# Performance work log

Hardware: AMD Instinct MI355X
Metric: run time of the kernel (lower is better)

The kernel has to match this reference:

```python
import jax, jax.numpy as jnp
import numpy as np

DIM = 512
HEADS = 8        # MultiHeadAttention default heads=8 (init 'heads' arg actually sets dim_head)
DIM_HEAD = 64    # from AttentionLayers heads=64 passed positionally as dim_head
HIDDEN = HEADS * DIM_HEAD  # 512
EPS = 1e-5


def setup_inputs() -> dict:
    key = jax.random.key(0)
    ks = jax.random.split(key, 8)
    s = 1.0 / np.sqrt(DIM)
    return {
        "x": jax.random.normal(ks[0], (4, 2048, DIM), dtype=jnp.float32),
        "ln_g": jnp.ones((DIM,), dtype=jnp.float32),
        "ln_b": jnp.zeros((DIM,), dtype=jnp.float32),
        "Wq": jax.random.normal(ks[1], (DIM, HIDDEN), dtype=jnp.float32) * s,
        "Wk": jax.random.normal(ks[2], (DIM, HIDDEN), dtype=jnp.float32) * s,
        "Wv": jax.random.normal(ks[3], (DIM, HIDDEN), dtype=jnp.float32) * s,
        "Wo": jax.random.normal(ks[4], (HIDDEN, DIM), dtype=jnp.float32) * s,
        "bo": jnp.zeros((DIM,), dtype=jnp.float32),
    }


def reference(x, ln_g, ln_b, Wq, Wk, Wv, Wo, bo):
    b, n, d = x.shape
    residual = x
    # pre-norm LayerNorm
    mu = jnp.mean(x, axis=-1, keepdims=True)
    var = jnp.mean((x - mu) ** 2, axis=-1, keepdims=True)
    xn = (x - mu) * jax.lax.rsqrt(var + EPS) * ln_g + ln_b
    # QKV projections (no bias), split into heads: [b, s, h, dh]
    q = (xn @ Wq).reshape(b, n, HEADS, DIM_HEAD)
    k = (xn @ Wk).reshape(b, n, HEADS, DIM_HEAD)
    v = (xn @ Wv).reshape(b, n, HEADS, DIM_HEAD)
    scale = HIDDEN ** (-0.5)  # note: scales by hidden_dim, not dim_head (faithful)
    scores = jnp.einsum('bihd,bjhd->bhij', q, k) * scale  # [b,h,i,j] full matrix
    attn = jax.nn.softmax(scores, axis=-1)
    out = jnp.einsum('bhij,bjhd->bihd', attn, v).reshape(b, n, HIDDEN)
    out = out @ Wo + bo
    # residual; the subsequent FFN layer's output is discarded in the source
    return out + residual
```

## Files before the change

kernel.cpp:

```cpp
#include <hip/hip_runtime.h>
#include <hip/hip_bf16.h>

#define DIM 512
#define SEQ 2048
#define BATCH 4
#define NHEADS 8
#define DH 64
#define NROWS (BATCH * SEQ)
#define LN_EPS 1e-5f

typedef __hip_bfloat16 bf16;
typedef __attribute__((ext_vector_type(8))) short short8;
typedef __attribute__((ext_vector_type(4))) float f32x4;

#define MFMA16(a, b, c) __builtin_amdgcn_mfma_f32_16x16x32_bf16((a), (b), (c), 0, 0, 0)

#if __has_builtin(__builtin_amdgcn_exp2f)
#define EXP2(x) __builtin_amdgcn_exp2f(x)
#else
#define EXP2(x) exp2f(x)
#endif

#if defined(__has_builtin)
#if __has_builtin(__builtin_amdgcn_global_load_lds)
#define HAS_GLDS 1
#endif
#endif

__device__ __forceinline__ void glds16(const bf16* g, bf16* l) {
#ifdef HAS_GLDS
  __builtin_amdgcn_global_load_lds((const __attribute__((address_space(1))) void*)g,
                                   (__attribute__((address_space(3))) void*)l, 16, 0, 0);
#else
  *reinterpret_cast<uint4*>(l) = *reinterpret_cast<const uint4*>(g);
#endif
}

__device__ __forceinline__ void store_bf16x4(bf16* p, float a, float b, float c, float d) {
  bf16 tmp[4] = {__float2bfloat16(a), __float2bfloat16(b), __float2bfloat16(c),
                 __float2bfloat16(d)};
  *reinterpret_cast<ushort4*>(p) = *reinterpret_cast<const ushort4*>(tmp);
}

#define B2F(us) __uint_as_float(((unsigned)(us)) << 16)

#define BARRIER() asm volatile("s_barrier" ::: "memory")
#define WAITVM0() asm volatile("s_waitcnt vmcnt(0)" ::: "memory")

#define Q_SCALE_LOG2E 0.06375872f

__global__ void setup_kernel(const float* __restrict__ x, const float* __restrict__ gamma,
                             const float* __restrict__ beta, bf16* __restrict__ xn,
                             const float* __restrict__ Wq, const float* __restrict__ Wk,
                             const float* __restrict__ Wv, const float* __restrict__ Wo,
                             bf16* __restrict__ Wt) {
  const int t = threadIdx.x;
  if (blockIdx.x < NROWS / 4) {
    const int row = blockIdx.x * 4 + (t >> 6);
    const int l = t & 63;
    const float4* xr = reinterpret_cast<const float4*>(x + (size_t)row * DIM);
    const float4 v0 = xr[l * 2];
    const float4 v1 = xr[l * 2 + 1];
    float s = (v0.x + v0.y + v0.z + v0.w) + (v1.x + v1.y + v1.z + v1.w);
    float ss = v0.x * v0.x + v0.y * v0.y + v0.z * v0.z + v0.w * v0.w + v1.x * v1.x +
               v1.y * v1.y + v1.z * v1.z + v1.w * v1.w;
#pragma unroll
    for (int off = 1; off < 64; off <<= 1) {
      s += __shfl_xor(s, off);
      ss += __shfl_xor(ss, off);
    }
    const float mu = s * (1.0f / DIM);
    const float rs = rsqrtf(ss * (1.0f / DIM) - mu * mu + LN_EPS);
    const float4 g0 = reinterpret_cast<const float4*>(gamma)[l * 2];
    const float4 g1 = reinterpret_cast<const float4*>(gamma)[l * 2 + 1];
    const float4 b0 = reinterpret_cast<const float4*>(beta)[l * 2];
    const float4 b1 = reinterpret_cast<const float4*>(beta)[l * 2 + 1];
    bf16* o = xn + (size_t)row * DIM + l * 8;
    store_bf16x4(o, (v0.x - mu) * rs * g0.x + b0.x, (v0.y - mu) * rs * g0.y + b0.y,
                 (v0.z - mu) * rs * g0.z + b0.z, (v0.w - mu) * rs * g0.w + b0.w);
    store_bf16x4(o + 4, (v1.x - mu) * rs * g1.x + b1.x, (v1.y - mu) * rs * g1.y + b1.y,
                 (v1.z - mu) * rs * g1.z + b1.z, (v1.w - mu) * rs * g1.w + b1.w);
  } else {
    __shared__ float tile[32][33];
    const int idx = blockIdx.x - NROWS / 4;
    const int bx = idx & 15, by = (idx >> 4) & 15, z = idx >> 8;
    const float* __restrict__ W = (z == 0) ? Wq : (z == 1) ? Wk : (z == 2) ? Wv : Wo;
    const float scale = (z == 0) ? Q_SCALE_LOG2E : 1.0f;
    bf16* __restrict__ dst = Wt + (size_t)z * DIM * DIM;
    const int tx = t & 31, ty = t >> 5;
#pragma unroll
    for (int i = 0; i < 32; i += 8)
      tile[ty + i][tx] = W[(size_t)(by * 32 + ty + i) * DIM + bx * 32 + tx];
    __syncthreads();
#pragma unroll
    for (int i = 0; i < 32; i += 8)
      dst[(size_t)(bx * 32 + ty + i) * DIM + by * 32 + tx] =
          __float2bfloat16(tile[tx][ty + i] * scale);
  }
}

__launch_bounds__(256, 3)
__global__ void gemm_qkv_kernel(const bf16* __restrict__ A, const bf16* __restrict__ Bt,
                                bf16* __restrict__ qo, bf16* __restrict__ ko,
                                bf16* __restrict__ vto) {
  const int m0 = blockIdx.x * 128, n0g = blockIdx.y * 128;
  __shared__ __align__(16) bf16 sA[2][128 * 32];
  __shared__ __align__(16) bf16 sB[2][128 * 32];
  const int t = threadIdx.x, w = t >> 6, l = t & 63;
  const int r = l & 15, g = l >> 4;
  const int wm = w >> 1, wn = w & 1;
  const int crow = w * 32 + (l >> 2);
  const int ccol = (l & 3) * 8;
  const bf16* gA = A + (size_t)(m0 + crow) * DIM + ccol;
  const bf16* gB = Bt + (size_t)(n0g + crow) * DIM + ccol;
  const int loff = l * 8;
  f32x4 acc[4][4] = {};
  glds16(gA, &sA[0][w * 1024 + loff]);
  glds16(gA + 16 * DIM, &sA[0][w * 1024 + loff + 512]);
  glds16(gB, &sB[0][w * 1024 + loff]);
  glds16(gB + 16 * DIM, &sB[0][w * 1024 + loff + 512]);
  const int NK = DIM / 32;
  const int z = n0g >> 9;
  const int b = m0 / SEQ;
  if (z != 2) {
    for (int ks = 0; ks < NK; ks++) {
      const int cur = ks & 1;
      __syncthreads();
      if (ks + 1 < NK) {
        const int k0n = (ks + 1) * 32;
        glds16(gA + k0n, &sA[1 - cur][w * 1024 + loff]);
        glds16(gA + 16 * DIM + k0n, &sA[1 - cur][w * 1024 + loff + 512]);
        glds16(gB + k0n, &sB[1 - cur][w * 1024 + loff]);
        glds16(gB + 16 * DIM + k0n, &sB[1 - cur][w * 1024 + loff + 512]);
      }
      short8 af[4], bfv[4];
#pragma unroll
      for (int i = 0; i < 4; i++)
        af[i] = *reinterpret_cast<const short8*>(&sA[cur][(wm * 64 + i * 16 + r) * 32 + g * 8]);
#pragma unroll
      for (int j = 0; j < 4; j++)
        bfv[j] = *reinterpret_cast<const short8*>(&sB[cur][(wn * 64 + j * 16 + r) * 32 + g * 8]);
#pragma unroll
      for (int i = 0; i < 4; i++)
#pragma unroll
        for (int j = 0; j < 4; j++) acc[i][j] = MFMA16(bfv[j], af[i], acc[i][j]);
    }
    bf16* __restrict__ outp = (z == 0) ? qo : ko;
    const int nc0 = (n0g & 511) + wn * 64;
#pragma unroll
    for (int i = 0; i < 4; i++) {
      const size_t mrow = (size_t)(m0 + wm * 64 + i * 16 + r) * DIM;
#pragma unroll
      for (int j = 0; j < 4; j++)
        store_bf16x4(outp + mrow + nc0 + j * 16 + g * 4, acc[i][j][0], acc[i][j][1],
                     acc[i][j][2], acc[i][j][3]);
    }
  } else {
    for (int ks = 0; ks < NK; ks++) {
      const int cur = ks & 1;
      __syncthreads();
      if (ks + 1 < NK) {
        const int k0n = (ks + 1) * 32;
        glds16(gA + k0n, &sA[1 - cur][w * 1024 + loff]);
        glds16(gA + 16 * DIM + k0n, &sA[1 - cur][w * 1024 + loff + 512]);
        glds16(gB + k0n, &sB[1 - cur][w * 1024 + loff]);
        glds16(gB + 16 * DIM + k0n, &sB[1 - cur][w * 1024 + loff + 512]);
      }
      short8 af[4], bfv[4];
#pragma unroll
      for (int i = 0; i < 4; i++)
        af[i] = *reinterpret_cast<const short8*>(&sA[cur][(wm * 64 + i * 16 + r) * 32 + g * 8]);
#pragma unroll
      for (int j = 0; j < 4; j++)
        bfv[j] = *reinterpret_cast<const short8*>(&sB[cur][(wn * 64 + j * 16 + r) * 32 + g * 8]);
#pragma unroll
      for (int i = 0; i < 4; i++)
#pragma unroll
        for (int j = 0; j < 4; j++) acc[i][j] = MFMA16(af[i], bfv[j], acc[i][j]);
    }
    const int nc0 = (n0g & 511) + wn * 64;
    const int seqbase = (m0 - b * SEQ) + wm * 64;
#pragma unroll
    for (int j = 0; j < 4; j++) {
      bf16* dst = vto + ((size_t)(b * DIM) + nc0 + j * 16 + r) * SEQ + seqbase + g * 4;
#pragma unroll
      for (int i = 0; i < 4; i++)
        store_bf16x4(dst + i * 16, acc[i][j][0], acc[i][j][1], acc[i][j][2], acc[i][j][3]);
    }
  }
}

template <bool SPLIT>
__launch_bounds__(256, 4)
__global__ void attn_kernel(const bf16* __restrict__ q, const bf16* __restrict__ k,
                            const bf16* __restrict__ vt, bf16* __restrict__ opart,
                            float* __restrict__ lpart) {
  const int bh = blockIdx.x, jh = blockIdx.y, it = blockIdx.z;
  const int b = bh >> 3, h = bh & 7;
  const int t = threadIdx.x, wv = t >> 6, l = t & 63;
  const int r = l & 15, g = l >> 4;
  __shared__ __align__(16) bf16 sK[2][32 * 64];
  __shared__ __align__(16) bf16 sV[2][64 * 32];
  __shared__ __align__(16) bf16 sPt[4][2][16][72];
  const int i0 = it * 128 + wv * 32;
  const bf16* qp = q + ((size_t)(b * SEQ) + i0 + r) * DIM + h * DH;
  short8 qf[2][2];
#pragma unroll
  for (int s = 0; s < 2; s++)
#pragma unroll
    for (int kc = 0; kc < 2; kc++)
      qf[s][kc] = *reinterpret_cast<const short8*>(qp + s * 16 * DIM + kc * 32 + g * 8);
  f32x4 oacc[2][4] = {};
  float lsum[2] = {0.f, 0.f};
  const int jbase = SPLIT ? jh * (SEQ / 2) : 0;
  const int kr8 = l >> 3;
  const int ku = ((l & 7) - kr8) & 7;
  const bf16* kg = k + ((size_t)(b * SEQ) + jbase + wv * 8 + kr8) * DIM + h * DH + ku * 8;
  const int vr4 = l >> 2;
  const int vu = ((l & 3) - ((l >> 3) & 3)) & 3;
  const bf16* vg = vt + ((size_t)(b * DIM) + h * DH + wv * 16 + vr4) * SEQ + jbase + vu * 8;
  const int loff = wv * 512 + l * 8;
  glds16(kg, &sK[0][loff]);
  glds16(vg, &sV[0][loff]);
  const int ek0 = r * 64 + 8 * ((g + r) & 7);
  const int ek1 = r * 64 + 8 * ((g + 4 + r) & 7);
  const int ev = r * 32 + 8 * ((g + (r >> 1)) & 3);
  const int NJ = (SPLIT ? SEQ / 2 : SEQ) / 32;
  for (int jt = 0; jt < NJ; jt++) {
    WAITVM0();
    BARRIER();
    if (jt + 1 < NJ) {
      const int j0n = (jt + 1) * 32;
      const int bn = (jt + 1) & 1;
      glds16(kg + (size_t)j0n * DIM, &sK[bn][loff]);
      glds16(vg + j0n, &sV[bn][loff]);
    }
    const bf16* sKb = sK[jt & 1];
    const bf16* sVb = sV[jt & 1];
    f32x4 st[2][2];
#pragma unroll
    for (int c = 0; c < 2; c++) {
      const short8 kf0 = *reinterpret_cast<const short8*>(sKb + 1024 * c + ek0);
      const short8 kf1 = *reinterpret_cast<const short8*>(sKb + 1024 * c + ek1);
#pragma unroll
      for (int s = 0; s < 2; s++) {
        f32x4 a = {0.f, 0.f, 0.f, 0.f};
        a = MFMA16(kf0, qf[s][0], a);
        a = MFMA16(kf1, qf[s][1], a);
        st[s][c] = a;
      }
    }
#pragma unroll
    for (int s = 0; s < 2; s++)
#pragma unroll
      for (int c = 0; c < 2; c++) {
        const float p0 = EXP2(st[s][c][0]);
        const float p1 = EXP2(st[s][c][1]);
        const float p2 = EXP2(st[s][c][2]);
        const float p3 = EXP2(st[s][c][3]);
        lsum[s] += (p0 + p1) + (p2 + p3);
        store_bf16x4(&sPt[wv][s][r][c * 16 + g * 4], p0, p1, p2, p3);
      }
    short8 pf[2];
#pragma unroll
    for (int s = 0; s < 2; s++)
      pf[s] = *reinterpret_cast<const short8*>(&sPt[wv][s][r][g * 8]);
#pragma unroll
    for (int dt = 0; dt < 4; dt++) {
      const short8 vf = *reinterpret_cast<const short8*>(sVb + 512 * dt + ev);
#pragma unroll
      for (int s = 0; s < 2; s++) oacc[s][dt] = MFMA16(vf, pf[s], oacc[s][dt]);
    }
  }
#pragma unroll
  for (int s = 0; s < 2; s++) {
    lsum[s] += __shfl_xor(lsum[s], 16);
    lsum[s] += __shfl_xor(lsum[s], 32);
  }
  const size_t obase = ((size_t)(SPLIT ? jh * 32 : 0) + bh) * SEQ;
#pragma unroll
  for (int s = 0; s < 2; s++) {
    const int i = i0 + s * 16 + r;
    if (l < 16) lpart[obase + i] = lsum[s];
#pragma unroll
    for (int dt = 0; dt < 4; dt++)
      store_bf16x4(opart + (obase + i) * 64 + dt * 16 + g * 4, oacc[s][dt][0], oacc[s][dt][1],
                   oacc[s][dt][2], oacc[s][dt][3]);
  }
  if (!SPLIT) {
    const size_t obase1 = ((size_t)32 + bh) * SEQ;
#pragma unroll
    for (int s = 0; s < 2; s++) {
      const int i = i0 + s * 16 + r;
      if (l < 16) lpart[obase1 + i] = 0.f;
#pragma unroll
      for (int dt = 0; dt < 4; dt++)
        store_bf16x4(opart + (obase1 + i) * 64 + dt * 16 + g * 4, 0.f, 0.f, 0.f, 0.f);
    }
  }
}

__launch_bounds__(256, 4)
__global__ void gemm_proj_kernel(const bf16* __restrict__ opart, const float* __restrict__ lpart,
                                 const bf16* __restrict__ Bt, const float* __restrict__ bo,
                                 const float* __restrict__ x, float* __restrict__ out) {
  const int m0 = blockIdx.x * 64, n0 = blockIdx.y * 128;
  __shared__ __align__(16) bf16 sA[64 * 32];
  __shared__ __align__(16) bf16 sB[128 * 32];
  const int t = threadIdx.x, w = t >> 6, l = t & 63;
  const int r = l & 15, g = l >> 4;
  const int wm = w >> 1, wn = w & 1;
  const int arow = t >> 2;
  const int acol = (t & 3) * 8;
  const bf16* gB = Bt + (size_t)(n0 + w * 32 + (l >> 2)) * DIM + (l & 3) * 8;
  f32x4 acc[2][4] = {};
  const int NK = DIM / 32;
  for (int ks = 0; ks < NK; ks++) {
    const int k0 = ks * 32;
    const int h = k0 >> 6;
    const int d0 = (k0 & 63) + acol;
    const int m = m0 + arow;
    const int bb = m >> 11, ii = m & 2047;
    const size_t row0 = ((size_t)(bb * 8 + h)) * SEQ + ii;
    const size_t row1 = row0 + (size_t)32 * SEQ;
    const uint4 A0 = *reinterpret_cast<const uint4*>(opart + row0 * 64 + d0);
    const uint4 A1 = *reinterpret_cast<const uint4*>(opart + row1 * 64 + d0);
    const float inv = 1.0f / (lpart[row0] + lpart[row1]);
    const ushort* a0 = (const ushort*)&A0;
    const ushort* a1 = (const ushort*)&A1;
    bf16 rr[8];
#pragma unroll
    for (int e = 0; e < 8; e++)
      rr[e] = __float2bfloat16((B2F(a0[e]) + B2F(a1[e])) * inv);
    const uint4 areg = *reinterpret_cast<const uint4*>(rr);
    __syncthreads();
    *reinterpret_cast<uint4*>(&sA[arow * 32 + acol]) = areg;
    glds16(gB + k0, sB + w * 1024 + l * 8);
    glds16(gB + 16 * DIM + k0, sB + w * 1024 + 512 + l * 8);
    __syncthreads();
    short8 af[2], bfv[4];
#pragma unroll
    for (int i = 0; i < 2; i++)
      af[i] = *reinterpret_cast<const short8*>(&sA[(wm * 32 + i * 16 + r) * 32 + g * 8]);
#pragma unroll
    for (int j = 0; j < 4; j++)
      bfv[j] = *reinterpret_cast<const short8*>(&sB[(wn * 64 + j * 16 + r) * 32 + g * 8]);
#pragma unroll
    for (int i = 0; i < 2; i++)
#pragma unroll
      for (int j = 0; j < 4; j++) acc[i][j] = MFMA16(bfv[j], af[i], acc[i][j]);
  }
#pragma unroll
  for (int i = 0; i < 2; i++) {
    const size_t mrow = (size_t)(m0 + wm * 32 + i * 16 + r) * DIM;
#pragma unroll
    for (int j = 0; j < 4; j++) {
      const int col0 = n0 + wn * 64 + j * 16 + g * 4;
      const float4 xb = *reinterpret_cast<const float4*>(x + mrow + col0);
      const float4 bb = *reinterpret_cast<const float4*>(bo + col0);
      float4 o;
      o.x = acc[i][j][0] + bb.x + xb.x;
      o.y = acc[i][j][1] + bb.y + xb.y;
      o.z = acc[i][j][2] + bb.z + xb.z;
      o.w = acc[i][j][3] + bb.w + xb.w;
      *reinterpret_cast<float4*>(out + mrow + col0) = o;
    }
  }
}

extern "C" void kernel_launch(void* const* d_in, const int* in_sizes, int n_in,
                              void* d_out, int out_size, void* d_ws, size_t ws_size,
                              hipStream_t stream) {
  (void)in_sizes; (void)n_in; (void)out_size;
  const float* x    = (const float*)d_in[0];
  const float* ln_g = (const float*)d_in[1];
  const float* ln_b = (const float*)d_in[2];
  const float* Wq   = (const float*)d_in[3];
  const float* Wk   = (const float*)d_in[4];
  const float* Wv   = (const float*)d_in[5];
  const float* Wo   = (const float*)d_in[6];
  const float* bo   = (const float*)d_in[7];
  float* out = (float*)d_out;
  char* ws = (char*)d_ws;
  bf16* xn  = (bf16*)(ws);
  bf16* wt  = (bf16*)(ws + (8u << 20));
  bf16* qb  = (bf16*)(ws + (10u << 20));
  bf16* kb  = (bf16*)(ws + (18u << 20));
  bf16* vtb = (bf16*)(ws + (26u << 20));
  bf16* opart = (bf16*)(ws + (34u << 20));
  float* lpart = (float*)(ws + (50u << 20));
  const bool split = ws_size >= ((50u << 20) + (1u << 19));

  setup_kernel<<<NROWS / 4 + 1024, 256, 0, stream>>>(x, ln_g, ln_b, xn, Wq, Wk, Wv, Wo, wt);
  gemm_qkv_kernel<<<dim3(NROWS / 128, (3 * DIM) / 128), 256, 0, stream>>>(xn, wt, qb, kb, vtb);
  if (split) {
    attn_kernel<true><<<dim3(BATCH * NHEADS, 2, SEQ / 128), 256, 0, stream>>>(
        qb, kb, vtb, opart, lpart);
  } else {
    attn_kernel<false><<<dim3(BATCH * NHEADS, 1, SEQ / 128), 256, 0, stream>>>(
        qb, kb, vtb, opart, lpart);
  }
  gemm_proj_kernel<<<dim3(NROWS / 64, DIM / 128), 256, 0, stream>>>(
      opart, lpart, wt + 3 * DIM * DIM, bo, x, out);
}
```

Baseline: 164.4 us.

## Triple-buffer QKV GEMM and double-buffer projection GEMM with register prefetch

The QKV GEMM moves from a double-buffered LDS pipeline to a triple-buffered one. It uses explicit vmcnt waits and one barrier per k-step, so global-to-LDS loads run two stages ahead. The output projection GEMM gains double-buffered LDS and register prefetch of the split-attention partials two steps ahead, with the combine written into the next buffer after the MFMAs. This drops one of its two barriers per k-step. The cost is more LDS per block, which may lower occupancy, and vmcnt counting that must stay correct for the glds instructions.

Measured after the change: 162.3 us. Within noise of the previous version (-1.3%).

```diff
diff --git a/kernel.cpp b/kernel.cpp
--- a/kernel.cpp
+++ b/kernel.cpp
@@ -46,6 +46,9 @@
 
 #define BARRIER() asm volatile("s_barrier" ::: "memory")
 #define WAITVM0() asm volatile("s_waitcnt vmcnt(0)" ::: "memory")
+#define WAITVM4() asm volatile("s_waitcnt vmcnt(4)" ::: "memory")
+#define WAITVM4_LGKM0() asm volatile("s_waitcnt vmcnt(4) lgkmcnt(0)" ::: "memory")
+#define WAITVM0_LGKM0() asm volatile("s_waitcnt vmcnt(0) lgkmcnt(0)" ::: "memory")
 
 #define Q_SCALE_LOG2E 0.06375872f
 
@@ -104,8 +107,8 @@
                                 bf16* __restrict__ qo, bf16* __restrict__ ko,
                                 bf16* __restrict__ vto) {
   const int m0 = blockIdx.x * 128, n0g = blockIdx.y * 128;
-  __shared__ __align__(16) bf16 sA[2][128 * 32];
-  __shared__ __align__(16) bf16 sB[2][128 * 32];
+  __shared__ __align__(16) bf16 sA[3][128 * 32];
+  __shared__ __align__(16) bf16 sB[3][128 * 32];
   const int t = threadIdx.x, w = t >> 6, l = t & 63;
   const int r = l & 15, g = l >> 4;
   const int wm = w >> 1, wn = w & 1;
@@ -113,26 +116,42 @@
   const int ccol = (l & 3) * 8;
   const bf16* gA = A + (size_t)(m0 + crow) * DIM + ccol;
   const bf16* gB = Bt + (size_t)(n0g + crow) * DIM + ccol;
-  const int loff = l * 8;
+  const int loff = w * 1024 + l * 8;
+  const int NK = DIM / 32;
+#define QKV_STAGE(dst, k0n)                             \
+  do {                                                  \
+    glds16(gA + (k0n), &sA[dst][loff]);                 \
+    glds16(gA + 16 * DIM + (k0n), &sA[dst][loff + 512]);\
+    glds16(gB + (k0n), &sB[dst][loff]);                 \
+    glds16(gB + 16 * DIM + (k0n), &sB[dst][loff + 512]);\
+  } while (0)
   f32x4 acc[4][4] = {};
-  glds16(gA, &sA[0][w * 1024 + loff]);
-  glds16(gA + 16 * DIM, &sA[0][w * 1024 + loff + 512]);
-  glds16(gB, &sB[0][w * 1024 + loff]);
-  glds16(gB + 16 * DIM, &sB[0][w * 1024 + loff + 512]);
-  const int NK = DIM / 32;
+  QKV_STAGE(0, 0);
+  QKV_STAGE(1, 32);
   const int z = n0g >> 9;
   const int b = m0 / SEQ;
   if (z != 2) {
-    for (int ks = 0; ks < NK; ks++) {
-      const int cur = ks & 1;
-      __syncthreads();
-      if (ks + 1 < NK) {
-        const int k0n = (ks + 1) * 32;
-        glds16(gA + k0n, &sA[1 - cur][w * 1024 + loff]);
-        glds16(gA + 16 * DIM + k0n, &sA[1 - cur][w * 1024 + loff + 512]);
-        glds16(gB + k0n, &sB[1 - cur][w * 1024 + loff]);
-        glds16(gB + 16 * DIM + k0n, &sB[1 - cur][w * 1024 + loff + 512]);
-      }
+    for (int ks = 0; ks < NK - 1; ks++) {
+      const int cur = ks % 3;
+      WAITVM4();
+      BARRIER();
+      if (ks + 2 < NK) QKV_STAGE((ks + 2) % 3, (ks + 2) * 32);
+      short8 af[4], bfv[4];
+#pragma unroll
+      for (int i = 0; i < 4; i++)
+        af[i] = *reinterpret_cast<const short8*>(&sA[cur][(wm * 64 + i * 16 + r) * 32 + g * 8]);
+#pragma unroll
+      for (int j = 0; j < 4; j++)
+        bfv[j] = *reinterpret_cast<const short8*>(&sB[cur][(wn * 64 + j * 16 + r) * 32 + g * 8]);
+#pragma unroll
+      for (int i = 0; i < 4; i++)
+#pragma unroll
+        for (int j = 0; j < 4; j++) acc[i][j] = MFMA16(bfv[j], af[i], acc[i][j]);
+    }
+    {
+      const int cur = (NK - 1) % 3;
+      WAITVM0();
+      BARRIER();
       short8 af[4], bfv[4];
 #pragma unroll
       for (int i = 0; i < 4; i++)
@@ -156,16 +175,11 @@
                      acc[i][j][2], acc[i][j][3]);
     }
   } else {
-    for (int ks = 0; ks < NK; ks++) {
-      const int cur = ks & 1;
-      __syncthreads();
-      if (ks + 1 < NK) {
-        const int k0n = (ks + 1) * 32;
-        glds16(gA + k0n, &sA[1 - cur][w * 1024 + loff]);
-        glds16(gA + 16 * DIM + k0n, &sA[1 - cur][w * 1024 + loff + 512]);
-        glds16(gB + k0n, &sB[1 - cur][w * 1024 + loff]);
-        glds16(gB + 16 * DIM + k0n, &sB[1 - cur][w * 1024 + loff + 512]);
-      }
+    for (int ks = 0; ks < NK - 1; ks++) {
+      const int cur = ks % 3;
+      WAITVM4();
+      BARRIER();
+      if (ks + 2 < NK) QKV_STAGE((ks + 2) % 3, (ks + 2) * 32);
       short8 af[4], bfv[4];
 #pragma unroll
       for (int i = 0; i < 4; i++)
@@ -178,6 +192,22 @@
 #pragma unroll
         for (int j = 0; j < 4; j++) acc[i][j] = MFMA16(af[i], bfv[j], acc[i][j]);
     }
+    {
+      const int cur = (NK - 1) % 3;
+      WAITVM0();
+      BARRIER();
+      short8 af[4], bfv[4];
+#pragma unroll
+      for (int i = 0; i < 4; i++)
+        af[i] = *reinterpret_cast<const short8*>(&sA[cur][(wm * 64 + i * 16 + r) * 32 + g * 8]);
+#pragma unroll
+      for (int j = 0; j < 4; j++)
+        bfv[j] = *reinterpret_cast<const short8*>(&sB[cur][(wn * 64 + j * 16 + r) * 32 + g * 8]);
+#pragma unroll
+      for (int i = 0; i < 4; i++)
+#pragma unroll
+        for (int j = 0; j < 4; j++) acc[i][j] = MFMA16(af[i], bfv[j], acc[i][j]);
+    }
     const int nc0 = (n0g & 511) + wn * 64;
     const int seqbase = (m0 - b * SEQ) + wm * 64;
 #pragma unroll
@@ -188,6 +218,7 @@
         store_bf16x4(dst + i * 16, acc[i][j][0], acc[i][j][1], acc[i][j][2], acc[i][j][3]);
     }
   }
+#undef QKV_STAGE
 }
 
 template <bool SPLIT>
@@ -300,56 +331,83 @@
   }
 }
 
+__device__ __forceinline__ void proj_combine_write(const uint4& A0, const uint4& A1,
+                                                   float l0, float l1, bf16* dst) {
+  const float inv = 1.0f / (l0 + l1);
+  const ushort* a0 = (const ushort*)&A0;
+  const ushort* a1 = (const ushort*)&A1;
+  bf16 rr[8];
+#pragma unroll
+  for (int e = 0; e < 8; e++)
+    rr[e] = __float2bfloat16((B2F(a0[e]) + B2F(a1[e])) * inv);
+  *reinterpret_cast<uint4*>(dst) = *reinterpret_cast<const uint4*>(rr);
+}
+
 __launch_bounds__(256, 4)
 __global__ void gemm_proj_kernel(const bf16* __restrict__ opart, const float* __restrict__ lpart,
                                  const bf16* __restrict__ Bt, const float* __restrict__ bo,
                                  const float* __restrict__ x, float* __restrict__ out) {
   const int m0 = blockIdx.x * 64, n0 = blockIdx.y * 128;
-  __shared__ __align__(16) bf16 sA[64 * 32];
-  __shared__ __align__(16) bf16 sB[128 * 32];
+  __shared__ __align__(16) bf16 sA[2][64 * 32];
+  __shared__ __align__(16) bf16 sB[2][128 * 32];
   const int t = threadIdx.x, w = t >> 6, l = t & 63;
   const int r = l & 15, g = l >> 4;
   const int wm = w >> 1, wn = w & 1;
   const int arow = t >> 2;
   const int acol = (t & 3) * 8;
   const bf16* gB = Bt + (size_t)(n0 + w * 32 + (l >> 2)) * DIM + (l & 3) * 8;
+  const int m = m0 + arow;
+  const int bb = m >> 11, ii = m & 2047;
+  const int NK = DIM / 32;
+#define PROJ_ALOAD(ks_)                                                   \
+  do {                                                                    \
+    const int h_ = (ks_) >> 1;                                            \
+    const int d0_ = (((ks_) * 32) & 63) + acol;                           \
+    const size_t row0_ = ((size_t)(bb * 8 + h_)) * SEQ + ii;              \
+    const size_t row1_ = row0_ + (size_t)32 * SEQ;                        \
+    A0p = *reinterpret_cast<const uint4*>(opart + row0_ * 64 + d0_);      \
+    A1p = *reinterpret_cast<const uint4*>(opart + row1_ * 64 + d0_);      \
+    l0p = lpart[row0_];                                                   \
+    l1p = lpart[row1_];                                                   \
+  } while (0)
+  uint4 A0p, A1p;
+  float l0p, l1p;
   f32x4 acc[2][4] = {};
-  const int NK = DIM / 32;
+  PROJ_ALOAD(0);
+  glds16(gB, &sB[0][w * 1024 + l * 8]);
+  glds16(gB + 16 * DIM, &sB[0][w * 1024 + 512 + l * 8]);
+  proj_combine_write(A0p, A1p, l0p, l1p, &sA[0][arow * 32 + acol]);
+  PROJ_ALOAD(1);
   for (int ks = 0; ks < NK; ks++) {
-    const int k0 = ks * 32;
-    const int h = k0 >> 6;
-    const int d0 = (k0 & 63) + acol;
-    const int m = m0 + arow;
-    const int bb = m >> 11, ii = m & 2047;
-    const size_t row0 = ((size_t)(bb * 8 + h)) * SEQ + ii;
-    const size_t row1 = row0 + (size_t)32 * SEQ;
-    const uint4 A0 = *reinterpret_cast<const uint4*>(opart + row0 * 64 + d0);
-    const uint4 A1 = *reinterpret_cast<const uint4*>(opart + row1 * 64 + d0);
-    const float inv = 1.0f / (lpart[row0] + lpart[row1]);
-    const ushort* a0 = (const ushort*)&A0;
-    const ushort* a1 = (const ushort*)&A1;
-    bf16 rr[8];
-#pragma unroll
-    for (int e = 0; e < 8; e++)
-      rr[e] = __float2bfloat16((B2F(a0[e]) + B2F(a1[e])) * inv);
-    const uint4 areg = *reinterpret_cast<const uint4*>(rr);
-    __syncthreads();
-    *reinterpret_cast<uint4*>(&sA[arow * 32 + acol]) = areg;
-    glds16(gB + k0, sB + w * 1024 + l * 8);
-    glds16(gB + 16 * DIM + k0, sB + w * 1024 + 512 + l * 8);
-    __syncthreads();
+    const int cur = ks & 1;
+    if (ks == NK - 1) {
+      WAITVM0_LGKM0();
+    } else {
+      WAITVM4_LGKM0();
+    }
+    BARRIER();
+    if (ks + 1 < NK) {
+      const int k0n = (ks + 1) * 32;
+      glds16(gB + k0n, &sB[1 - cur][w * 1024 + l * 8]);
+      glds16(gB + 16 * DIM + k0n, &sB[1 - cur][w * 1024 + 512 + l * 8]);
+    }
     short8 af[2], bfv[4];
 #pragma unroll
     for (int i = 0; i < 2; i++)
-      af[i] = *reinterpret_cast<const short8*>(&sA[(wm * 32 + i * 16 + r) * 32 + g * 8]);
+      af[i] = *reinterpret_cast<const short8*>(&sA[cur][(wm * 32 + i * 16 + r) * 32 + g * 8]);
 #pragma unroll
     for (int j = 0; j < 4; j++)
-      bfv[j] = *reinterpret_cast<const short8*>(&sB[(wn * 64 + j * 16 + r) * 32 + g * 8]);
+      bfv[j] = *reinterpret_cast<const short8*>(&sB[cur][(wn * 64 + j * 16 + r) * 32 + g * 8]);
 #pragma unroll
     for (int i = 0; i < 2; i++)
 #pragma unroll
       for (int j = 0; j < 4; j++) acc[i][j] = MFMA16(bfv[j], af[i], acc[i][j]);
-  }
+    if (ks + 1 < NK) {
+      proj_combine_write(A0p, A1p, l0p, l1p, &sA[1 - cur][arow * 32 + acol]);
+      if (ks + 2 < NK) PROJ_ALOAD(ks + 2);
+    }
+  }
+#undef PROJ_ALOAD
 #pragma unroll
   for (int i = 0; i < 2; i++) {
     const size_t mrow = (size_t)(m0 + wm * 32 + i * 16 + r) * DIM;
@@ -357,12 +415,12 @@
     for (int j = 0; j < 4; j++) {
       const int col0 = n0 + wn * 64 + j * 16 + g * 4;
       const float4 xb = *reinterpret_cast<const float4*>(x + mrow + col0);
-      const float4 bb = *reinterpret_cast<const float4*>(bo + col0);
+      const float4 bb2 = *reinterpret_cast<const float4*>(bo + col0);
       float4 o;
-      o.x = acc[i][j][0] + bb.x + xb.x;
-      o.y = acc[i][j][1] + bb.y + xb.y;
-      o.z = acc[i][j][2] + bb.z + xb.z;
-      o.w = acc[i][j][3] + bb.w + xb.w;
+      o.x = acc[i][j][0] + bb2.x + xb.x;
+      o.y = acc[i][j][1] + bb2.y + xb.y;
+      o.z = acc[i][j][2] + bb2.z + xb.z;
+      o.w = acc[i][j][3] + bb2.w + xb.w;
       *reinterpret_cast<float4*>(out + mrow + col0) = o;
     }
   }
```
